# Kernel optimization log

Hardware: AMD Instinct MI355X
Metric: run time of the kernel (lower is better)

The kernel has to match this reference:

```python
import jax, jax.numpy as jnp
import numpy as np

B, NQ, NK = 16, 512, 1024
CQ, CV = 128, 128
H, D = 8, 64            # nb_heads, attention_size
SCALE = float(np.sqrt(D))


def setup_inputs() -> dict:
    key = jax.random.key(0)
    ks = jax.random.split(key, 10)
    s = 0.02
    return {
        "query": jax.random.normal(ks[0], (B, NQ, CQ), jnp.float32),
        "key": jax.random.normal(ks[1], (B, NK, CV), jnp.float32),
        "c_mask": jax.random.randint(ks[2], (B, NK), 0, 2).astype(jnp.float32),
        # torch Linear params, stored as [in, out] so y = x @ W + b
        "Wq": jax.random.normal(ks[3], (CQ, H * D), jnp.float32) * s,
        "bq": jnp.zeros((H * D,), jnp.float32),
        "Wk": jax.random.normal(ks[4], (CV, H * D), jnp.float32) * s,
        "bk": jnp.zeros((H * D,), jnp.float32),
        "Wv": jax.random.normal(ks[5], (CV, H * D), jnp.float32) * s,
        "bv": jnp.zeros((H * D,), jnp.float32),
    }


def reference(query, key, c_mask, Wq, bq, Wk, bk, Wv, bv):
    # projections -> [B, N, H, D]
    q = (query @ Wq + bq).reshape(B, NQ, H, D)
    k = (key @ Wk + bk).reshape(B, NK, H, D)
    v = (key @ Wv + bv).reshape(B, NK, H, D)
    # scaled scores [B, H, NQ, NK]
    scores = jnp.einsum('bqhd,bkhd->bhqk', q / SCALE, k)
    # additive mask: c_mask [B, NK] broadcasts over heads and queries
    scores = scores - 100000.0 * (1.0 - c_mask[:, None, None, :])
    attn = jax.nn.softmax(scores, axis=-1)
    # weighted values -> [B, NQ, H, D] -> concat heads
    c = jnp.einsum('bhqk,bkhd->bqhd', attn, v)
    return c.reshape(B, NQ, H * D)
```

## Files before the change

### kernel.cpp

```cpp
#include <hip/hip_runtime.h>
#include <hip/hip_bf16.h>

#define B_  16
#define NQ_ 512
#define NK_ 1024
#define CQ_ 128
#define H_  8
#define D_  64
#define HD_ 512

typedef __attribute__((ext_vector_type(8))) short short8;
typedef __attribute__((ext_vector_type(4))) float floatx4;

__device__ __forceinline__ short f2bf(float f) {
    union { float f; unsigned u; } x; x.f = f;
    unsigned r = (x.u + 0x7fffu + ((x.u >> 16) & 1u)) >> 16;
    return (short)r;
}
__device__ __forceinline__ int f2bf_pk(float a, float b) {
    __hip_bfloat162 h = __float22bfloat162_rn(make_float2(a, b));
    int r; __builtin_memcpy(&r, &h, 4); return r;
}
__device__ __forceinline__ short8 pack8(float4 a, float4 b) {
    union { int4 i; short8 s; } u;
    u.i = make_int4(f2bf_pk(a.x, a.y), f2bf_pk(a.z, a.w),
                    f2bf_pk(b.x, b.y), f2bf_pk(b.z, b.w));
    return u.s;
}
__device__ __forceinline__ int2 packi2(floatx4 a) {
    return make_int2(f2bf_pk(a[0], a[1]), f2bf_pk(a[2], a[3]));
}

__global__ void prep_kernel(const float* __restrict__ W0, const float* __restrict__ W1,
                            const float* __restrict__ W2, short* __restrict__ T0,
                            short* __restrict__ T1, short* __restrict__ T2,
                            const float* __restrict__ bq, float* __restrict__ bqs,
                            float qscale) {
    int gi = blockIdx.x * blockDim.x + threadIdx.x;
    if (gi < 196608) {
        int sel = gi >> 16;
        int idx = gi & 65535;
        const float* W = sel == 0 ? W0 : (sel == 1 ? W1 : W2);
        short* T = sel == 0 ? T0 : (sel == 1 ? T1 : T2);
        float s = sel == 0 ? qscale : 1.0f;
        int n = idx >> 7, k = idx & 127;
        T[idx] = f2bf(W[k * HD_ + n] * s);
        return;
    }
    int j = gi - 196608;
    if (j < HD_) bqs[j] = bq[j] * qscale;
}

__global__ __launch_bounds__(512, 2) void fused_kernel(
    const float* __restrict__ query, const float* __restrict__ key_,
    const float* __restrict__ cmask,
    const short* __restrict__ wqt, const short* __restrict__ wkt,
    const short* __restrict__ wvt,
    const float* __restrict__ bqs, const float* __restrict__ bk,
    const float* __restrict__ bv, float* __restrict__ out)
{
    __shared__ __align__(16) short ksh[2][64 * 72];
    __shared__ __align__(16) short vsh[2][64 * 72];
    __shared__ __align__(16) short psh[256 * 72];

    const int tid = threadIdx.x;
    const int w = tid >> 6, lane = tid & 63;
    const int l15 = lane & 15, quad = lane >> 4;

    const int bx     = blockIdx.x;
    const int bh_i   = bx & 127;
    const int qhalf  = bx >> 7;
    const int h      = bh_i & 7;
    const int b      = bh_i >> 3;

    const float* xkey = key_ + (size_t)b * NK_ * CQ_;
    const float* mk   = cmask + (size_t)b * NK_;

    const short* Wkv = (w < 4) ? wkt : wvt;
    const int nt = w & 3;

    short8 qa[2][2];
    {
        short8 waf[4][4];
        #pragma unroll
        for (int dt = 0; dt < 4; ++dt)
            #pragma unroll
            for (int kt = 0; kt < 4; ++kt)
                waf[dt][kt] = *(const short8*)(wqt + (size_t)(h * 64 + dt * 16 + l15) * CQ_ + kt * 32 + quad * 8);
        const int qr0 = qhalf * 256 + w * 32;
        #pragma unroll
        for (int g = 0; g < 2; ++g) {
            const float* qrow = query + ((size_t)b * NQ_ + qr0 + g * 16 + l15) * CQ_;
            short8 bqf[4];
            #pragma unroll
            for (int kt = 0; kt < 4; ++kt)
                bqf[kt] = pack8(*(const float4*)(qrow + kt * 32 + quad * 8),
                                *(const float4*)(qrow + kt * 32 + quad * 8 + 4));
            const int prow = (w * 32 + g * 16 + l15) * 72;
            #pragma unroll
            for (int dt = 0; dt < 4; ++dt) {
                float4 bi = *(const float4*)(bqs + h * 64 + dt * 16 + quad * 4);
                floatx4 a = {bi.x, bi.y, bi.z, bi.w};
                #pragma unroll
                for (int kt = 0; kt < 4; ++kt)
                    a = __builtin_amdgcn_mfma_f32_16x16x32_bf16(waf[dt][kt], bqf[kt], a, 0, 0, 0);
                *(int2*)&psh[prow + dt * 16 + quad * 4] = packi2(a);
            }
            qa[g][0] = *(const short8*)&psh[prow + quad * 8];
            qa[g][1] = *(const short8*)&psh[prow + 32 + quad * 8];
        }
    }

    float l_lane[2] = {0.f, 0.f};
    floatx4 o_acc[2][4];
    #pragma unroll
    for (int g = 0; g < 2; ++g)
        #pragma unroll
        for (int dt = 0; dt < 4; ++dt) o_acc[g][dt] = (floatx4){0.f, 0.f, 0.f, 0.f};

    auto proj_mfma_write = [&](const short8 xf[4], const short8 wf[4][4], int bufi) {
        if (w < 4) {
            #pragma unroll
            for (int dt = 0; dt < 4; ++dt) {
                float4 bi = *(const float4*)(bk + h * 64 + dt * 16 + quad * 4);
                floatx4 a = {bi.x, bi.y, bi.z, bi.w};
                #pragma unroll
                for (int kt = 0; kt < 4; ++kt)
                    a = __builtin_amdgcn_mfma_f32_16x16x32_bf16(wf[dt][kt], xf[kt], a, 0, 0, 0);
                *(int2*)&ksh[bufi][(nt * 16 + l15) * 72 + dt * 16 + quad * 4] = packi2(a);
            }
        } else {
            #pragma unroll
            for (int dt = 0; dt < 4; ++dt) {
                const float bvv = bv[h * 64 + dt * 16 + l15];
                floatx4 a = {bvv, bvv, bvv, bvv};
                #pragma unroll
                for (int kt = 0; kt < 4; ++kt)
                    a = __builtin_amdgcn_mfma_f32_16x16x32_bf16(xf[kt], wf[dt][kt], a, 0, 0, 0);
                *(int2*)&vsh[bufi][(dt * 16 + l15) * 72 + nt * 16 + quad * 4] = packi2(a);
            }
        }
    };
    auto load_xf = [&](int kbase, short8 xf[4]) {
        const float* krow = xkey + (size_t)(kbase + nt * 16 + l15) * CQ_;
        #pragma unroll
        for (int kt = 0; kt < 4; ++kt)
            xf[kt] = pack8(*(const float4*)(krow + kt * 32 + quad * 8),
                           *(const float4*)(krow + kt * 32 + quad * 8 + 4));
    };
    auto load_wf = [&](short8 wf[4][4]) {
        #pragma unroll
        for (int dt = 0; dt < 4; ++dt)
            #pragma unroll
            for (int kt = 0; kt < 4; ++kt)
                wf[dt][kt] = *(const short8*)(Wkv + (size_t)(h * 64 + dt * 16 + l15) * CQ_ + kt * 32 + quad * 8);
    };

    {
        short8 xf[4], wf[4][4];
        load_xf(0, xf);
        load_wf(wf);
        proj_mfma_write(xf, wf, 0);
    }
    __syncthreads();

    for (int t = 0; t < 16; ++t) {
        const int cur = t & 1;
        const int kbase = t * 64;

        short8 xf[4];
        if (t < 15) load_xf(kbase + 64, xf);

        float4 m4[4];
        #pragma unroll
        for (int n2 = 0; n2 < 4; ++n2)
            m4[n2] = *(const float4*)(mk + kbase + n2 * 16 + quad * 4);

        short8 ka[4][2];
        #pragma unroll
        for (int n2 = 0; n2 < 4; ++n2) {
            ka[n2][0] = *(const short8*)&ksh[cur][(n2 * 16 + l15) * 72 + quad * 8];
            ka[n2][1] = *(const short8*)&ksh[cur][(n2 * 16 + l15) * 72 + 32 + quad * 8];
        }
        short8 vf[2][4];
        #pragma unroll
        for (int dt = 0; dt < 4; ++dt) {
            vf[0][dt] = *(const short8*)&vsh[cur][(dt * 16 + l15) * 72 + quad * 8];
            vf[1][dt] = *(const short8*)&vsh[cur][(dt * 16 + l15) * 72 + 32 + quad * 8];
        }

        #pragma unroll
        for (int g = 0; g < 2; ++g) {
            floatx4 st[4];
            #pragma unroll
            for (int n2 = 0; n2 < 4; ++n2) {
                floatx4 a = {0.f, 0.f, 0.f, 0.f};
                a = __builtin_amdgcn_mfma_f32_16x16x32_bf16(ka[n2][1], qa[g][1], a, 0, 0, 0);
                a = __builtin_amdgcn_mfma_f32_16x16x32_bf16(ka[n2][0], qa[g][0], a, 0, 0, 0);
                st[n2] = a;
            }
            const int prow = (w * 32 + g * 16 + l15) * 72;
            float psum = 0.f;
            #pragma unroll
            for (int n2 = 0; n2 < 4; ++n2) {
                float p0 = m4[n2].x * __builtin_amdgcn_exp2f(st[n2][0]);
                float p1 = m4[n2].y * __builtin_amdgcn_exp2f(st[n2][1]);
                float p2 = m4[n2].z * __builtin_amdgcn_exp2f(st[n2][2]);
                float p3 = m4[n2].w * __builtin_amdgcn_exp2f(st[n2][3]);
                psum += (p0 + p1) + (p2 + p3);
                *(int2*)&psh[prow + n2 * 16 + quad * 4] =
                    make_int2(f2bf_pk(p0, p1), f2bf_pk(p2, p3));
            }
            l_lane[g] += psum;
            #pragma unroll
            for (int kt = 0; kt < 2; ++kt) {
                short8 pa = *(const short8*)&psh[prow + kt * 32 + quad * 8];
                #pragma unroll
                for (int dt = 0; dt < 4; ++dt)
                    o_acc[g][dt] = __builtin_amdgcn_mfma_f32_16x16x32_bf16(vf[kt][dt], pa, o_acc[g][dt], 0, 0, 0);
            }
        }

        if (t < 15) {
            short8 wf[4][4];
            load_wf(wf);
            proj_mfma_write(xf, wf, cur ^ 1);
        }
        __syncthreads();
    }

    #pragma unroll
    for (int g = 0; g < 2; ++g) {
        float ls = l_lane[g];
        ls += __shfl_xor(ls, 16);
        ls += __shfl_xor(ls, 32);
        const float linv = 1.0f / ls;
        const int qr = qhalf * 256 + w * 32 + g * 16 + l15;
        float* orow = out + ((size_t)b * NQ_ + qr) * HD_ + h * D_;
        #pragma unroll
        for (int dt = 0; dt < 4; ++dt) {
            float4 v = make_float4(o_acc[g][dt][0] * linv, o_acc[g][dt][1] * linv,
                                   o_acc[g][dt][2] * linv, o_acc[g][dt][3] * linv);
            *(float4*)(orow + dt * 16 + quad * 4) = v;
        }
    }
}

extern "C" void kernel_launch(void* const* d_in, const int* in_sizes, int n_in,
                              void* d_out, int out_size, void* d_ws, size_t ws_size,
                              hipStream_t stream) {
    const float* query = (const float*)d_in[0];
    const float* key   = (const float*)d_in[1];
    const float* cmask = (const float*)d_in[2];
    const float* Wq    = (const float*)d_in[3];
    const float* bq    = (const float*)d_in[4];
    const float* Wk    = (const float*)d_in[5];
    const float* bk    = (const float*)d_in[6];
    const float* Wv    = (const float*)d_in[7];
    const float* bv    = (const float*)d_in[8];
    float* out = (float*)d_out;

    char* ws = (char*)d_ws;
    short* wqt = (short*)(ws);
    short* wkt = (short*)(ws + 131072);
    short* wvt = (short*)(ws + 131072 * 2);
    float* bqs = (float*)(ws + 131072 * 3);

    const float qscale = 0.125f * 1.44269504f;
    prep_kernel<<<dim3(771), dim3(256), 0, stream>>>(
        Wq, Wk, Wv, wqt, wkt, wvt, bq, bqs, qscale);

    fused_kernel<<<dim3(256), dim3(512), 0, stream>>>(
        query, key, cmask, wqt, wkt, wvt, bqs, bk, bv, out);
}
```

Baseline: 160.3 us.

## Split blocks to 128 queries with 4 waves, swizzle LDS, keep weights in registers

Each block now handles 128 query rows with 256 threads instead of 256 rows with 512, so the grid doubles to 512 blocks. Each wave projects two 16-row key/value tiles per step. The K/V weight fragments and biases are loaded once into registers and no longer reloaded every iteration. LDS tiles drop the 72-element padding in favour of an XOR swizzle on 16-byte chunks, which shrinks shared memory and is meant to avoid bank conflicts. The cost is that K/V projection is now recomputed by twice as many blocks, and the weights held in registers raise register pressure.

```diff
diff --git a/kernel.cpp b/kernel.cpp
--- a/kernel.cpp
+++ b/kernel.cpp
@@ -51,7 +51,7 @@
     if (j < HD_) bqs[j] = bq[j] * qscale;
 }
 
-__global__ __launch_bounds__(512, 2) void fused_kernel(
+__global__ __launch_bounds__(256, 2) void fused_kernel(
     const float* __restrict__ query, const float* __restrict__ key_,
     const float* __restrict__ cmask,
     const short* __restrict__ wqt, const short* __restrict__ wkt,
@@ -59,25 +59,26 @@
     const float* __restrict__ bqs, const float* __restrict__ bk,
     const float* __restrict__ bv, float* __restrict__ out)
 {
-    __shared__ __align__(16) short ksh[2][64 * 72];
-    __shared__ __align__(16) short vsh[2][64 * 72];
-    __shared__ __align__(16) short psh[256 * 72];
+    __shared__ __align__(16) short ksh[2][64 * 64];
+    __shared__ __align__(16) short vsh[2][64 * 64];
+    __shared__ __align__(16) short psh[128 * 64];
 
     const int tid = threadIdx.x;
     const int w = tid >> 6, lane = tid & 63;
     const int l15 = lane & 15, quad = lane >> 4;
 
-    const int bx     = blockIdx.x;
-    const int bh_i   = bx & 127;
-    const int qhalf  = bx >> 7;
-    const int h      = bh_i & 7;
-    const int b      = bh_i >> 3;
+    const int bx   = blockIdx.x;
+    const int bh_i = bx & 127;
+    const int qq   = bx >> 7;
+    const int h    = bh_i & 7;
+    const int b    = bh_i >> 3;
 
     const float* xkey = key_ + (size_t)b * NK_ * CQ_;
     const float* mk   = cmask + (size_t)b * NK_;
 
-    const short* Wkv = (w < 4) ? wkt : wvt;
-    const int nt = w & 3;
+    const int kv  = w >> 1;
+    const int sub = w & 1;
+    const short* Wkv = kv ? wvt : wkt;
 
     short8 qa[2][2];
     {
@@ -87,7 +88,7 @@
             #pragma unroll
             for (int kt = 0; kt < 4; ++kt)
                 waf[dt][kt] = *(const short8*)(wqt + (size_t)(h * 64 + dt * 16 + l15) * CQ_ + kt * 32 + quad * 8);
-        const int qr0 = qhalf * 256 + w * 32;
+        const int qr0 = qq * 128 + w * 32;
         #pragma unroll
         for (int g = 0; g < 2; ++g) {
             const float* qrow = query + ((size_t)b * NQ_ + qr0 + g * 16 + l15) * CQ_;
@@ -96,7 +97,7 @@
             for (int kt = 0; kt < 4; ++kt)
                 bqf[kt] = pack8(*(const float4*)(qrow + kt * 32 + quad * 8),
                                 *(const float4*)(qrow + kt * 32 + quad * 8 + 4));
-            const int prow = (w * 32 + g * 16 + l15) * 72;
+            const int prow = w * 32 + g * 16 + l15;
             #pragma unroll
             for (int dt = 0; dt < 4; ++dt) {
                 float4 bi = *(const float4*)(bqs + h * 64 + dt * 16 + quad * 4);
@@ -104,12 +105,68 @@
                 #pragma unroll
                 for (int kt = 0; kt < 4; ++kt)
                     a = __builtin_amdgcn_mfma_f32_16x16x32_bf16(waf[dt][kt], bqf[kt], a, 0, 0, 0);
-                *(int2*)&psh[prow + dt * 16 + quad * 4] = packi2(a);
-            }
-            qa[g][0] = *(const short8*)&psh[prow + quad * 8];
-            qa[g][1] = *(const short8*)&psh[prow + 32 + quad * 8];
-        }
-    }
+                const int c16 = (dt * 2 + (quad >> 1)) ^ (prow & 7);
+                *(int2*)&psh[prow * 64 + c16 * 8 + (quad & 1) * 4] = packi2(a);
+            }
+            qa[g][0] = *(const short8*)&psh[prow * 64 + ((quad    ) ^ (prow & 7)) * 8];
+            qa[g][1] = *(const short8*)&psh[prow * 64 + ((4 + quad) ^ (prow & 7)) * 8];
+        }
+    }
+
+    short8 wf[4][4];
+    #pragma unroll
+    for (int dt = 0; dt < 4; ++dt)
+        #pragma unroll
+        for (int kt = 0; kt < 4; ++kt)
+            wf[dt][kt] = *(const short8*)(Wkv + (size_t)(h * 64 + dt * 16 + l15) * CQ_ + kt * 32 + quad * 8);
+    float4 bk4[4];
+    float  bv4[4];
+    #pragma unroll
+    for (int dt = 0; dt < 4; ++dt) {
+        if (kv == 0) bk4[dt] = *(const float4*)(bk + h * 64 + dt * 16 + quad * 4);
+        else         bv4[dt] = bv[h * 64 + dt * 16 + l15];
+    }
+
+    auto load_x2 = [&](int kbase, short8 xf[2][4]) {
+        #pragma unroll
+        for (int j = 0; j < 2; ++j) {
+            const int nt = sub * 2 + j;
+            const float* krow = xkey + (size_t)(kbase + nt * 16 + l15) * CQ_;
+            #pragma unroll
+            for (int kt = 0; kt < 4; ++kt)
+                xf[j][kt] = pack8(*(const float4*)(krow + kt * 32 + quad * 8),
+                                  *(const float4*)(krow + kt * 32 + quad * 8 + 4));
+        }
+    };
+    auto proj_write = [&](short8 xf[2][4], int bufi) {
+        #pragma unroll
+        for (int j = 0; j < 2; ++j) {
+            const int nt = sub * 2 + j;
+            if (kv == 0) {
+                #pragma unroll
+                for (int dt = 0; dt < 4; ++dt) {
+                    floatx4 a = {bk4[dt].x, bk4[dt].y, bk4[dt].z, bk4[dt].w};
+                    #pragma unroll
+                    for (int kt = 0; kt < 4; ++kt)
+                        a = __builtin_amdgcn_mfma_f32_16x16x32_bf16(wf[dt][kt], xf[j][kt], a, 0, 0, 0);
+                    const int r = nt * 16 + l15;
+                    const int c16 = (dt * 2 + (quad >> 1)) ^ (r & 7);
+                    *(int2*)&ksh[bufi][r * 64 + c16 * 8 + (quad & 1) * 4] = packi2(a);
+                }
+            } else {
+                #pragma unroll
+                for (int dt = 0; dt < 4; ++dt) {
+                    floatx4 a = {bv4[dt], bv4[dt], bv4[dt], bv4[dt]};
+                    #pragma unroll
+                    for (int kt = 0; kt < 4; ++kt)
+                        a = __builtin_amdgcn_mfma_f32_16x16x32_bf16(xf[j][kt], wf[dt][kt], a, 0, 0, 0);
+                    const int r = dt * 16 + l15;
+                    const int c16 = (nt * 2 + (quad >> 1)) ^ (r & 7);
+                    *(int2*)&vsh[bufi][r * 64 + c16 * 8 + (quad & 1) * 4] = packi2(a);
+                }
+            }
+        }
+    };
 
     float l_lane[2] = {0.f, 0.f};
     floatx4 o_acc[2][4];
@@ -118,49 +175,10 @@
         #pragma unroll
         for (int dt = 0; dt < 4; ++dt) o_acc[g][dt] = (floatx4){0.f, 0.f, 0.f, 0.f};
 
-    auto proj_mfma_write = [&](const short8 xf[4], const short8 wf[4][4], int bufi) {
-        if (w < 4) {
-            #pragma unroll
-            for (int dt = 0; dt < 4; ++dt) {
-                float4 bi = *(const float4*)(bk + h * 64 + dt * 16 + quad * 4);
-                floatx4 a = {bi.x, bi.y, bi.z, bi.w};
-                #pragma unroll
-                for (int kt = 0; kt < 4; ++kt)
-                    a = __builtin_amdgcn_mfma_f32_16x16x32_bf16(wf[dt][kt], xf[kt], a, 0, 0, 0);
-                *(int2*)&ksh[bufi][(nt * 16 + l15) * 72 + dt * 16 + quad * 4] = packi2(a);
-            }
-        } else {
-            #pragma unroll
-            for (int dt = 0; dt < 4; ++dt) {
-                const float bvv = bv[h * 64 + dt * 16 + l15];
-                floatx4 a = {bvv, bvv, bvv, bvv};
-                #pragma unroll
-                for (int kt = 0; kt < 4; ++kt)
-                    a = __builtin_amdgcn_mfma_f32_16x16x32_bf16(xf[kt], wf[dt][kt], a, 0, 0, 0);
-                *(int2*)&vsh[bufi][(dt * 16 + l15) * 72 + nt * 16 + quad * 4] = packi2(a);
-            }
-        }
-    };
-    auto load_xf = [&](int kbase, short8 xf[4]) {
-        const float* krow = xkey + (size_t)(kbase + nt * 16 + l15) * CQ_;
-        #pragma unroll
-        for (int kt = 0; kt < 4; ++kt)
-            xf[kt] = pack8(*(const float4*)(krow + kt * 32 + quad * 8),
-                           *(const float4*)(krow + kt * 32 + quad * 8 + 4));
-    };
-    auto load_wf = [&](short8 wf[4][4]) {
-        #pragma unroll
-        for (int dt = 0; dt < 4; ++dt)
-            #pragma unroll
-            for (int kt = 0; kt < 4; ++kt)
-                wf[dt][kt] = *(const short8*)(Wkv + (size_t)(h * 64 + dt * 16 + l15) * CQ_ + kt * 32 + quad * 8);
-    };
-
     {
-        short8 xf[4], wf[4][4];
-        load_xf(0, xf);
-        load_wf(wf);
-        proj_mfma_write(xf, wf, 0);
+        short8 xf0[2][4];
+        load_x2(0, xf0);
+        proj_write(xf0, 0);
     }
     __syncthreads();
 
@@ -168,8 +186,8 @@
         const int cur = t & 1;
         const int kbase = t * 64;
 
-        short8 xf[4];
-        if (t < 15) load_xf(kbase + 64, xf);
+        short8 xfn[2][4];
+        if (t < 15) load_x2(kbase + 64, xfn);
 
         float4 m4[4];
         #pragma unroll
@@ -179,14 +197,16 @@
         short8 ka[4][2];
         #pragma unroll
         for (int n2 = 0; n2 < 4; ++n2) {
-            ka[n2][0] = *(const short8*)&ksh[cur][(n2 * 16 + l15) * 72 + quad * 8];
-            ka[n2][1] = *(const short8*)&ksh[cur][(n2 * 16 + l15) * 72 + 32 + quad * 8];
+            const int r = n2 * 16 + l15;
+            ka[n2][0] = *(const short8*)&ksh[cur][r * 64 + ((quad    ) ^ (r & 7)) * 8];
+            ka[n2][1] = *(const short8*)&ksh[cur][r * 64 + ((4 + quad) ^ (r & 7)) * 8];
         }
         short8 vf[2][4];
         #pragma unroll
         for (int dt = 0; dt < 4; ++dt) {
-            vf[0][dt] = *(const short8*)&vsh[cur][(dt * 16 + l15) * 72 + quad * 8];
-            vf[1][dt] = *(const short8*)&vsh[cur][(dt * 16 + l15) * 72 + 32 + quad * 8];
+            const int r = dt * 16 + l15;
+            vf[0][dt] = *(const short8*)&vsh[cur][r * 64 + ((quad    ) ^ (r & 7)) * 8];
+            vf[1][dt] = *(const short8*)&vsh[cur][r * 64 + ((4 + quad) ^ (r & 7)) * 8];
         }
 
         #pragma unroll
@@ -199,7 +219,7 @@
                 a = __builtin_amdgcn_mfma_f32_16x16x32_bf16(ka[n2][0], qa[g][0], a, 0, 0, 0);
                 st[n2] = a;
             }
-            const int prow = (w * 32 + g * 16 + l15) * 72;
+            const int prow = w * 32 + g * 16 + l15;
             float psum = 0.f;
             #pragma unroll
             for (int n2 = 0; n2 < 4; ++n2) {
@@ -208,24 +228,21 @@
                 float p2 = m4[n2].z * __builtin_amdgcn_exp2f(st[n2][2]);
                 float p3 = m4[n2].w * __builtin_amdgcn_exp2f(st[n2][3]);
                 psum += (p0 + p1) + (p2 + p3);
-                *(int2*)&psh[prow + n2 * 16 + quad * 4] =
+                const int c16 = (2 * n2 + (quad >> 1)) ^ (prow & 7);
+                *(int2*)&psh[prow * 64 + c16 * 8 + (quad & 1) * 4] =
                     make_int2(f2bf_pk(p0, p1), f2bf_pk(p2, p3));
             }
             l_lane[g] += psum;
             #pragma unroll
             for (int kt = 0; kt < 2; ++kt) {
-                short8 pa = *(const short8*)&psh[prow + kt * 32 + quad * 8];
+                short8 pa = *(const short8*)&psh[prow * 64 + ((kt * 4 + quad) ^ (prow & 7)) * 8];
                 #pragma unroll
                 for (int dt = 0; dt < 4; ++dt)
                     o_acc[g][dt] = __builtin_amdgcn_mfma_f32_16x16x32_bf16(vf[kt][dt], pa, o_acc[g][dt], 0, 0, 0);
             }
         }
 
-        if (t < 15) {
-            short8 wf[4][4];
-            load_wf(wf);
-            proj_mfma_write(xf, wf, cur ^ 1);
-        }
+        if (t < 15) proj_write(xfn, cur ^ 1);
         __syncthreads();
     }
 
@@ -235,7 +252,7 @@
         ls += __shfl_xor(ls, 16);
         ls += __shfl_xor(ls, 32);
         const float linv = 1.0f / ls;
-        const int qr = qhalf * 256 + w * 32 + g * 16 + l15;
+        const int qr = qq * 128 + w * 32 + g * 16 + l15;
         float* orow = out + ((size_t)b * NQ_ + qr) * HD_ + h * D_;
         #pragma unroll
         for (int dt = 0; dt < 4; ++dt) {
@@ -270,6 +287,6 @@
     prep_kernel<<<dim3(771), dim3(256), 0, stream>>>(
         Wq, Wk, Wv, wqt, wkt, wvt, bq, bqs, qscale);
 
-    fused_kernel<<<dim3(256), dim3(512), 0, stream>>>(
+    fused_kernel<<<dim3(512), dim3(256), 0, stream>>>(
         query, key, cmask, wqt, wkt, wvt, bqs, bk, bv, out);
 }
```

Measured after the change: 203.2 us. +26.7%, slower.
